# Kernel optimization log

Measured on AMD Instinct MI355X. Metric: run time of the kernel, lower is better.

The kernel has to match this reference:

```python
import jax, jax.numpy as jnp
import numpy as np
from jax import lax

N = 25600      # total nodes = G * T
E = 204800     # edges (before self loops)
IN_CH = 6
HID = 64
HEADS = 4
G = 512        # graphs per batch
T = 50         # sequence length (node_time in [0, T))
OUT = 30       # prediction_horizon * 3
NEG_SLOPE = 0.2
BN_EPS = 1e-5


def _gat(x, src, dst, W, a_src, a_dst, b, heads, outc):
    # PyG GATConv (concat=True): h = x W reshaped to (N, H, C)
    n = x.shape[0]
    h = (x @ W).reshape(n, heads, outc)
    # edge scores: leaky_relu(a_src . h_src + a_dst . h_dst), softmax over incoming edges of dst
    e = jax.nn.leaky_relu((h * a_src).sum(-1)[src] + (h * a_dst).sum(-1)[dst], NEG_SLOPE)  # (E, H)
    m = jax.ops.segment_max(e, dst, num_segments=n)
    ex = jnp.exp(e - m[dst])
    denom = jax.ops.segment_sum(ex, dst, num_segments=n)
    alpha = ex / denom[dst]
    out = jax.ops.segment_sum(alpha[:, :, None] * h[src], dst, num_segments=n)  # (N, H, C)
    return out.reshape(n, heads * outc) + b


def _bn_eval(x, g, b):
    # BatchNorm in eval with running_mean=0, running_var=1
    return g * (x * (1.0 / np.float32(np.sqrt(1.0 + BN_EPS)))) + b


def setup_inputs() -> dict:
    ks = jax.random.split(jax.random.key(0), 16)
    s = 0.1
    d = {}
    d["x"] = jax.random.normal(ks[0], (N, IN_CH), jnp.float32)
    d["edge_index"] = jax.random.randint(ks[1], (2, E), 0, N)
    idx = jnp.arange(N)
    d["batch"] = idx // T       # each graph has exactly T nodes
    d["node_time"] = idx % T
    d["W1"] = jax.random.normal(ks[2], (IN_CH, HEADS * HID), jnp.float32) * s
    d["att_src1"] = jax.random.normal(ks[3], (HEADS, HID), jnp.float32) * s
    d["att_dst1"] = jax.random.normal(ks[4], (HEADS, HID), jnp.float32) * s
    d["b1"] = jnp.zeros((HEADS * HID,), jnp.float32)
    d["g1"] = jnp.ones((HEADS * HID,), jnp.float32)
    d["be1"] = jnp.zeros((HEADS * HID,), jnp.float32)
    d["W2"] = jax.random.normal(ks[5], (HEADS * HID, HID), jnp.float32) * s
    d["att_src2"] = jax.random.normal(ks[6], (1, HID), jnp.float32) * s
    d["att_dst2"] = jax.random.normal(ks[7], (1, HID), jnp.float32) * s
    d["b2"] = jnp.zeros((HID,), jnp.float32)
    d["g2"] = jnp.ones((HID,), jnp.float32)
    d["be2"] = jnp.zeros((HID,), jnp.float32)
    d["Wih"] = jax.random.normal(ks[8], (4 * HID, HID), jnp.float32) * s
    d["Whh"] = jax.random.normal(ks[9], (4 * HID, HID), jnp.float32) * s
    d["bih"] = jnp.zeros((4 * HID,), jnp.float32)
    d["bhh"] = jnp.zeros((4 * HID,), jnp.float32)
    d["Wfc"] = jax.random.normal(ks[10], (HID, OUT), jnp.float32) * s
    d["bfc"] = jnp.zeros((OUT,), jnp.float32)
    return d


def reference(x, edge_index, batch, node_time, W1, att_src1, att_dst1, b1, g1, be1,
              W2, att_src2, att_dst2, b2, g2, be2, Wih, Whh, bih, bhh, Wfc, bfc):
    loops = jnp.arange(N)
    src = jnp.concatenate([edge_index[0], loops])  # GATConv adds self loops
    dst = jnp.concatenate([edge_index[1], loops])
    h = jax.nn.elu(_bn_eval(_gat(x, src, dst, W1, att_src1, att_dst1, b1, HEADS, HID), g1, be1))
    h = jax.nn.elu(_bn_eval(_gat(h, src, dst, W2, att_src2, att_dst2, b2, 1, HID), g2, be2))
    # vectorized replacement of the per-node python scatter loop
    x_seq = jnp.zeros((G, T, HID), h.dtype).at[batch, node_time].set(h)

    def step(carry, xt):
        hh, cc = carry
        gates = xt @ Wih.T + bih + hh @ Whh.T + bhh
        i, f, gg, o = jnp.split(gates, 4, axis=-1)
        cc = jax.nn.sigmoid(f) * cc + jax.nn.sigmoid(i) * jnp.tanh(gg)
        hh = jax.nn.sigmoid(o) * jnp.tanh(cc)
        return (hh, cc), None

    init = (jnp.zeros((G, HID), h.dtype), jnp.zeros((G, HID), h.dtype))
    (hn, _), _ = lax.scan(step, init, x_seq.transpose(1, 0, 2))  # scan over time
    return hn @ Wfc + bfc  # (G, 30)
```

## Files before the change

### kernel.cpp

```cpp
#include <hip/hip_runtime.h>

#define N_NODES 25600
#define N_EDGES 204800
#define EE (N_EDGES + N_NODES)
#define IN_CH 6
#define HID 64
#define HEADS 4
#define G_GRAPHS 512
#define T_STEPS 50
#define OUT_DIM 30
#define NEG_SLOPE 0.2f
#define BN_INV 0.9999950000374997f

__device__ __forceinline__ float lrelu_(float x){ return x > 0.f ? x : NEG_SLOPE * x; }
__device__ __forceinline__ float elu_(float x){ return x > 0.f ? x : __expf(x) - 1.f; }
__device__ __forceinline__ float sigmoid_(float x){ return 1.f / (1.f + __expf(-x)); }

__global__ void count_k(const int* __restrict__ ei, int* __restrict__ counts){
    int e = blockIdx.x * 256 + threadIdx.x;
    if (e >= EE) return;
    int dst = (e < N_EDGES) ? ei[N_EDGES + e] : (e - N_EDGES);
    atomicAdd(&counts[dst], 1);
}

__global__ void scan_k(const int* __restrict__ counts, int* __restrict__ row_ptr,
                       int* __restrict__ cursor){
    __shared__ int part[1024];
    int t = threadIdx.x;
    const int CH = N_NODES / 1024;
    int base = t * CH;
    int s = 0;
    for (int i = 0; i < CH; i++) s += counts[base + i];
    part[t] = s;
    __syncthreads();
    for (int off = 1; off < 1024; off <<= 1){
        int v = (t >= off) ? part[t - off] : 0;
        __syncthreads();
        part[t] += v;
        __syncthreads();
    }
    int run = (t > 0) ? part[t - 1] : 0;
    for (int i = 0; i < CH; i++){
        int cv = counts[base + i];
        row_ptr[base + i] = run;
        cursor[base + i]  = run;
        run += cv;
    }
    if (t == 1023) row_ptr[N_NODES] = run;
}

__global__ void scatter_k(const int* __restrict__ ei, int* __restrict__ cursor,
                          int* __restrict__ ssrc){
    int e = blockIdx.x * 256 + threadIdx.x;
    if (e >= EE) return;
    int src, dst;
    if (e < N_EDGES){ src = ei[e]; dst = ei[N_EDGES + e]; }
    else            { src = dst = e - N_EDGES; }
    int pos = atomicAdd(&cursor[dst], 1);
    ssrc[pos] = src;
}

__global__ void gat1_tr(const float* __restrict__ x, const float* __restrict__ W1,
                        const float* __restrict__ asw, const float* __restrict__ adw,
                        float* __restrict__ h1_pre, float* __restrict__ as1,
                        float* __restrict__ ad1){
    __shared__ float w[IN_CH * 256];
    int tid = threadIdx.x;
    for (int i = tid; i < IN_CH * 256; i += 256) w[i] = W1[i];
    __syncthreads();
    int wv = tid >> 6, lane = tid & 63;
    int n = blockIdx.x * 4 + wv;
    float xv[IN_CH];
    #pragma unroll
    for (int k = 0; k < IN_CH; k++) xv[k] = x[n * IN_CH + k];
    float sA[4], sD[4];
    #pragma unroll
    for (int h = 0; h < 4; h++){
        int col = h * 64 + lane;
        float acc = 0.f;
        #pragma unroll
        for (int k = 0; k < IN_CH; k++) acc += xv[k] * w[k * 256 + col];
        h1_pre[n * 256 + col] = acc;
        sA[h] = acc * asw[col];
        sD[h] = acc * adw[col];
    }
    #pragma unroll
    for (int h = 0; h < 4; h++){
        #pragma unroll
        for (int off = 32; off; off >>= 1){
            sA[h] += __shfl_xor(sA[h], off);
            sD[h] += __shfl_xor(sD[h], off);
        }
    }
    if (lane == 0){
        *(float4*)&as1[n * 4] = make_float4(sA[0], sA[1], sA[2], sA[3]);
        *(float4*)&ad1[n * 4] = make_float4(sD[0], sD[1], sD[2], sD[3]);
    }
}

__global__ void gat1_agg(const float* __restrict__ h1_pre, const float* __restrict__ as1,
                         const float* __restrict__ ad1, const int* __restrict__ row_ptr,
                         const int* __restrict__ ssrc,
                         const float* __restrict__ b1, const float* __restrict__ g1,
                         const float* __restrict__ be1, float* __restrict__ h1_act){
    int wv = threadIdx.x >> 6, lane = threadIdx.x & 63;
    int n = blockIdx.x * 4 + wv;
    int s0 = row_ptr[n], s1 = row_ptr[n + 1];
    float4 adn = *(const float4*)&ad1[n * 4];
    float d0 = 0.f, d1 = 0.f, d2 = 0.f, d3 = 0.f;
    float a0 = 0.f, a1 = 0.f, a2 = 0.f, a3 = 0.f;
    for (int j = s0; j < s1; j++){
        int s = ssrc[j];
        float4 as = *(const float4*)&as1[s * 4];
        float e0 = __expf(lrelu_(as.x + adn.x));
        float e1 = __expf(lrelu_(as.y + adn.y));
        float e2 = __expf(lrelu_(as.z + adn.z));
        float e3 = __expf(lrelu_(as.w + adn.w));
        d0 += e0; d1 += e1; d2 += e2; d3 += e3;
        const float* hp = h1_pre + (size_t)s * 256;
        a0 += e0 * hp[lane];
        a1 += e1 * hp[64 + lane];
        a2 += e2 * hp[128 + lane];
        a3 += e3 * hp[192 + lane];
    }
    float accs[4] = {a0 / d0, a1 / d1, a2 / d2, a3 / d3};
    #pragma unroll
    for (int h = 0; h < 4; h++){
        int col = h * 64 + lane;
        float v = accs[h] + b1[col];
        v = g1[col] * (v * BN_INV) + be1[col];
        h1_act[(size_t)n * 256 + col] = elu_(v);
    }
}

#define TM 64
#define KT 32
#define APAD 4
__global__ __launch_bounds__(256) void gat2_tr(const float* __restrict__ h1_act,
                        const float* __restrict__ W2,
                        const float* __restrict__ asw, const float* __restrict__ adw,
                        float* __restrict__ h2_pre, float* __restrict__ as2,
                        float* __restrict__ ad2){
    __shared__ float As[TM][KT + APAD];
    __shared__ float Bs[KT][64];
    int tx = threadIdx.x;
    int rg = tx >> 4;
    int cg = tx & 15;
    int r0 = rg * 4, c0 = cg * 4;
    int rowBase = blockIdx.x * TM;
    float acc[4][4] = {};
    for (int k0 = 0; k0 < 256; k0 += KT){
        #pragma unroll
        for (int it = 0; it < 2; it++){
            int i = tx + it * 256;
            int row = i >> 3;
            int c4  = (i & 7) * 4;
            *(float4*)&As[row][c4] =
                *(const float4*)(h1_act + (size_t)(rowBase + row) * 256 + k0 + c4);
        }
        #pragma unroll
        for (int it = 0; it < 2; it++){
            int i = tx + it * 256;
            int row = i >> 4;
            int c4  = (i & 15) * 4;
            *(float4*)&Bs[row][c4] = *(const float4*)(W2 + (size_t)(k0 + row) * 64 + c4);
        }
        __syncthreads();
        #pragma unroll
        for (int kq = 0; kq < KT; kq += 4){
            float4 b0 = *(float4*)&Bs[kq + 0][c0];
            float4 b1v = *(float4*)&Bs[kq + 1][c0];
            float4 b2v = *(float4*)&Bs[kq + 2][c0];
            float4 b3 = *(float4*)&Bs[kq + 3][c0];
            #pragma unroll
            for (int i = 0; i < 4; i++){
                float4 a = *(float4*)&As[r0 + i][kq];
                acc[i][0] += a.x * b0.x + a.y * b1v.x + a.z * b2v.x + a.w * b3.x;
                acc[i][1] += a.x * b0.y + a.y * b1v.y + a.z * b2v.y + a.w * b3.y;
                acc[i][2] += a.x * b0.z + a.y * b1v.z + a.z * b2v.z + a.w * b3.z;
                acc[i][3] += a.x * b0.w + a.y * b1v.w + a.z * b2v.w + a.w * b3.w;
            }
        }
        __syncthreads();
    }
    float aw0 = asw[c0], aw1 = asw[c0+1], aw2 = asw[c0+2], aw3 = asw[c0+3];
    float dw0 = adw[c0], dw1 = adw[c0+1], dw2 = adw[c0+2], dw3 = adw[c0+3];
    #pragma unroll
    for (int i = 0; i < 4; i++){
        int row = rowBase + r0 + i;
        *(float4*)(h2_pre + (size_t)row * 64 + c0) =
            make_float4(acc[i][0], acc[i][1], acc[i][2], acc[i][3]);
        float sA = acc[i][0]*aw0 + acc[i][1]*aw1 + acc[i][2]*aw2 + acc[i][3]*aw3;
        float sD = acc[i][0]*dw0 + acc[i][1]*dw1 + acc[i][2]*dw2 + acc[i][3]*dw3;
        #pragma unroll
        for (int off = 8; off; off >>= 1){
            sA += __shfl_xor(sA, off);
            sD += __shfl_xor(sD, off);
        }
        if (cg == 0){ as2[row] = sA; ad2[row] = sD; }
    }
}

__global__ void gat2_agg(const float* __restrict__ h2_pre, const float* __restrict__ as2,
                         const float* __restrict__ ad2, const int* __restrict__ row_ptr,
                         const int* __restrict__ ssrc,
                         const float* __restrict__ b2, const float* __restrict__ g2,
                         const float* __restrict__ be2,
                         const int* __restrict__ batch, const int* __restrict__ ntime,
                         float* __restrict__ xseq){
    int wv = threadIdx.x >> 6, lane = threadIdx.x & 63;
    int n = blockIdx.x * 4 + wv;
    int s0 = row_ptr[n], s1 = row_ptr[n + 1];
    float adn = ad2[n];
    float denom = 0.f, acc = 0.f;
    for (int j = s0; j < s1; j++){
        int s = ssrc[j];
        float e = __expf(lrelu_(as2[s] + adn));
        denom += e;
        acc += e * h2_pre[(size_t)s * 64 + lane];
    }
    float v = acc / denom + b2[lane];
    v = g2[lane] * (v * BN_INV) + be2[lane];
    v = elu_(v);
    int pos = batch[n] * T_STEPS + ntime[n];
    xseq[(size_t)pos * 64 + lane] = v;
}

__global__ __launch_bounds__(256, 2) void lstm_k(const float* __restrict__ xseq,
        const float* __restrict__ Wih, const float* __restrict__ Whh,
        const float* __restrict__ bih, const float* __restrict__ bhh,
        const float* __restrict__ Wfc, const float* __restrict__ bfc,
        float* __restrict__ out){
    int g = blockIdx.x;
    int j = threadIdx.x;
    __shared__ float4 xt4[16];
    __shared__ float4 h4[16];
    __shared__ float gates[256];
    float4 wih[16], whh[16];
    const float4* Wr = (const float4*)(Wih + j * 64);
    const float4* Hr = (const float4*)(Whh + j * 64);
    #pragma unroll
    for (int k = 0; k < 16; k++){ wih[k] = Wr[k]; whh[k] = Hr[k]; }
    float bsum = bih[j] + bhh[j];
    float c = 0.f;
    if (j < 16) h4[j] = make_float4(0.f, 0.f, 0.f, 0.f);
    __syncthreads();
    const float4* xg = (const float4*)(xseq + (size_t)g * T_STEPS * 64);
    for (int t = 0; t < T_STEPS; t++){
        if (j < 16) xt4[j] = xg[t * 16 + j];
        __syncthreads();
        float acc = bsum;
        #pragma unroll
        for (int k = 0; k < 16; k++){
            float4 xv = xt4[k]; float4 wv = wih[k];
            acc += wv.x * xv.x; acc += wv.y * xv.y;
            acc += wv.z * xv.z; acc += wv.w * xv.w;
            float4 hv = h4[k]; float4 wh = whh[k];
            acc += wh.x * hv.x; acc += wh.y * hv.y;
            acc += wh.z * hv.z; acc += wh.w * hv.w;
        }
        gates[j] = acc;
        __syncthreads();
        if (j < 64){
            float iv = gates[j], fv = gates[64 + j], gv = gates[128 + j], ov = gates[192 + j];
            c = sigmoid_(fv) * c + sigmoid_(iv) * tanhf(gv);
            float hn = sigmoid_(ov) * tanhf(c);
            ((float*)h4)[j] = hn;
        }
        __syncthreads();
    }
    if (j < OUT_DIM){
        float acc = bfc[j];
        const float* hf = (const float*)h4;
        #pragma unroll
        for (int k = 0; k < 64; k++) acc += hf[k] * Wfc[k * OUT_DIM + j];
        out[g * OUT_DIM + j] = acc;
    }
}

extern "C" void kernel_launch(void* const* d_in, const int* in_sizes, int n_in,
                              void* d_out, int out_size, void* d_ws, size_t ws_size,
                              hipStream_t stream){
    const float* x    = (const float*)d_in[0];
    const int*   ei   = (const int*)  d_in[1];
    const int*   batch= (const int*)  d_in[2];
    const int*   ntime= (const int*)  d_in[3];
    const float* W1   = (const float*)d_in[4];
    const float* as1w = (const float*)d_in[5];
    const float* ad1w = (const float*)d_in[6];
    const float* b1   = (const float*)d_in[7];
    const float* g1   = (const float*)d_in[8];
    const float* be1  = (const float*)d_in[9];
    const float* W2   = (const float*)d_in[10];
    const float* as2w = (const float*)d_in[11];
    const float* ad2w = (const float*)d_in[12];
    const float* b2   = (const float*)d_in[13];
    const float* g2   = (const float*)d_in[14];
    const float* be2  = (const float*)d_in[15];
    const float* Wih  = (const float*)d_in[16];
    const float* Whh  = (const float*)d_in[17];
    const float* bih  = (const float*)d_in[18];
    const float* bhh  = (const float*)d_in[19];
    const float* Wfc  = (const float*)d_in[20];
    const float* bfc  = (const float*)d_in[21];
    float* out = (float*)d_out;

    char* w = (char*)d_ws;
    auto alloc = [&](size_t bytes)->char*{
        char* p = w;
        w += (bytes + 255) & ~size_t(255);
        return p;
    };
    float* h1_pre = (float*)alloc((size_t)N_NODES * 256 * 4);
    float* h1_act = (float*)alloc((size_t)N_NODES * 256 * 4);
    float* h2_pre = (float*)alloc((size_t)N_NODES * 64 * 4);
    float* xseq   = (float*)alloc((size_t)G_GRAPHS * T_STEPS * 64 * 4);
    float* as1    = (float*)alloc((size_t)N_NODES * 4 * 4);
    float* ad1    = (float*)alloc((size_t)N_NODES * 4 * 4);
    float* as2    = (float*)alloc((size_t)N_NODES * 4);
    float* ad2    = (float*)alloc((size_t)N_NODES * 4);
    int* counts   = (int*)alloc((size_t)N_NODES * 4);
    int* row_ptr  = (int*)alloc((size_t)(N_NODES + 1) * 4);
    int* cursor   = (int*)alloc((size_t)N_NODES * 4);
    int* ssrc     = (int*)alloc((size_t)EE * 4);

    hipMemsetAsync(counts, 0, (size_t)N_NODES * 4, stream);
    count_k  <<<(EE + 255) / 256, 256, 0, stream>>>(ei, counts);
    scan_k   <<<1, 1024, 0, stream>>>(counts, row_ptr, cursor);
    scatter_k<<<(EE + 255) / 256, 256, 0, stream>>>(ei, cursor, ssrc);
    gat1_tr  <<<N_NODES / 4, 256, 0, stream>>>(x, W1, as1w, ad1w, h1_pre, as1, ad1);
    gat1_agg <<<N_NODES / 4, 256, 0, stream>>>(h1_pre, as1, ad1, row_ptr, ssrc, b1, g1, be1, h1_act);
    gat2_tr  <<<N_NODES / TM, 256, 0, stream>>>(h1_act, W2, as2w, ad2w, h2_pre, as2, ad2);
    gat2_agg <<<N_NODES / 4, 256, 0, stream>>>(h2_pre, as2, ad2, row_ptr, ssrc, b2, g2, be2, batch, ntime, xseq);
    lstm_k   <<<G_GRAPHS, 256, 0, stream>>>(xseq, Wih, Whh, bih, bhh, Wfc, bfc, out);
}
```

Measured before the change: 315.4 us.

## Hoist LSTM input projection into a separate batched GEMM kernel

Computes x_t·Wih^T plus both biases for all timesteps up front in a tiled shared-memory GEMM and writes the result into the reused h1_pre buffer. The recurrent kernel then only does the Whh product each step, which removes one barrier per step and half the per-step FMAs and weight registers. In exchange it adds an extra kernel launch and a write and read of a 25600x256 float intermediate. Sigmoid also switches to a fast division.

Result: no change. 320.0 us (+1.4%).

```diff
diff --git a/kernel.cpp b/kernel.cpp
--- a/kernel.cpp
+++ b/kernel.cpp
@@ -14,7 +14,7 @@
 
 __device__ __forceinline__ float lrelu_(float x){ return x > 0.f ? x : NEG_SLOPE * x; }
 __device__ __forceinline__ float elu_(float x){ return x > 0.f ? x : __expf(x) - 1.f; }
-__device__ __forceinline__ float sigmoid_(float x){ return 1.f / (1.f + __expf(-x)); }
+__device__ __forceinline__ float sigmoid_(float x){ return __fdividef(1.f, 1.f + __expf(-x)); }
 
 __global__ void count_k(const int* __restrict__ ei, int* __restrict__ counts){
     int e = blockIdx.x * 256 + threadIdx.x;
@@ -226,35 +226,79 @@
     xseq[(size_t)pos * 64 + lane] = v;
 }
 
-__global__ __launch_bounds__(256, 2) void lstm_k(const float* __restrict__ xseq,
-        const float* __restrict__ Wih, const float* __restrict__ Whh,
-        const float* __restrict__ bih, const float* __restrict__ bhh,
-        const float* __restrict__ Wfc, const float* __restrict__ bfc,
-        float* __restrict__ out){
+__global__ __launch_bounds__(256) void xproj_k(const float* __restrict__ xseq,
+        const float* __restrict__ Wih, const float* __restrict__ bih,
+        const float* __restrict__ bhh, float* __restrict__ xproj){
+    __shared__ float As[64][68];
+    __shared__ float Bs[64][64];
+    int tx = threadIdx.x;
+    int bx = blockIdx.x;
+    int m0 = (bx >> 2) * 64, n0 = (bx & 3) * 64;
+    #pragma unroll
+    for (int it = 0; it < 4; it++){
+        int i = tx + it * 256;
+        int r = i >> 4, c4 = (i & 15) * 4;
+        *(float4*)&As[r][c4] = *(const float4*)(xseq + (size_t)(m0 + r) * 64 + c4);
+    }
+    #pragma unroll
+    for (int it = 0; it < 4; it++){
+        int i = tx + it * 256;
+        int n = i & 63, k4 = (i >> 6) * 4;
+        float4 w = *(const float4*)(Wih + (size_t)(n0 + n) * 64 + k4);
+        Bs[k4 + 0][n] = w.x; Bs[k4 + 1][n] = w.y;
+        Bs[k4 + 2][n] = w.z; Bs[k4 + 3][n] = w.w;
+    }
+    __syncthreads();
+    int rg = tx >> 4, cg = tx & 15;
+    int r0 = rg * 4, c0 = cg * 4;
+    float acc[4][4] = {};
+    #pragma unroll
+    for (int k4 = 0; k4 < 16; k4++){
+        int k = k4 * 4;
+        float4 b0 = *(float4*)&Bs[k + 0][c0];
+        float4 b1v = *(float4*)&Bs[k + 1][c0];
+        float4 b2v = *(float4*)&Bs[k + 2][c0];
+        float4 b3 = *(float4*)&Bs[k + 3][c0];
+        #pragma unroll
+        for (int i = 0; i < 4; i++){
+            float4 a = *(float4*)&As[r0 + i][k];
+            acc[i][0] += a.x * b0.x + a.y * b1v.x + a.z * b2v.x + a.w * b3.x;
+            acc[i][1] += a.x * b0.y + a.y * b1v.y + a.z * b2v.y + a.w * b3.y;
+            acc[i][2] += a.x * b0.z + a.y * b1v.z + a.z * b2v.z + a.w * b3.z;
+            acc[i][3] += a.x * b0.w + a.y * b1v.w + a.z * b2v.w + a.w * b3.w;
+        }
+    }
+    float bb0 = bih[n0 + c0 + 0] + bhh[n0 + c0 + 0];
+    float bb1 = bih[n0 + c0 + 1] + bhh[n0 + c0 + 1];
+    float bb2 = bih[n0 + c0 + 2] + bhh[n0 + c0 + 2];
+    float bb3 = bih[n0 + c0 + 3] + bhh[n0 + c0 + 3];
+    #pragma unroll
+    for (int i = 0; i < 4; i++){
+        int row = m0 + r0 + i;
+        *(float4*)(xproj + (size_t)row * 256 + n0 + c0) =
+            make_float4(acc[i][0] + bb0, acc[i][1] + bb1, acc[i][2] + bb2, acc[i][3] + bb3);
+    }
+}
+
+__global__ __launch_bounds__(256, 2) void lstm3_k(const float* __restrict__ xproj,
+        const float* __restrict__ Whh, const float* __restrict__ Wfc,
+        const float* __restrict__ bfc, float* __restrict__ out){
     int g = blockIdx.x;
     int j = threadIdx.x;
-    __shared__ float4 xt4[16];
     __shared__ float4 h4[16];
     __shared__ float gates[256];
-    float4 wih[16], whh[16];
-    const float4* Wr = (const float4*)(Wih + j * 64);
-    const float4* Hr = (const float4*)(Whh + j * 64);
-    #pragma unroll
-    for (int k = 0; k < 16; k++){ wih[k] = Wr[k]; whh[k] = Hr[k]; }
-    float bsum = bih[j] + bhh[j];
+    float4 whh[16];
+    const float4* Hr = (const float4*)(Whh + (size_t)j * 64);
+    #pragma unroll
+    for (int k = 0; k < 16; k++) whh[k] = Hr[k];
     float c = 0.f;
     if (j < 16) h4[j] = make_float4(0.f, 0.f, 0.f, 0.f);
     __syncthreads();
-    const float4* xg = (const float4*)(xseq + (size_t)g * T_STEPS * 64);
+    const float* xp = xproj + (size_t)g * T_STEPS * 256;
     for (int t = 0; t < T_STEPS; t++){
-        if (j < 16) xt4[j] = xg[t * 16 + j];
-        __syncthreads();
-        float acc = bsum;
+        float acc = xp[t * 256 + j];
         #pragma unroll
         for (int k = 0; k < 16; k++){
-            float4 xv = xt4[k]; float4 wv = wih[k];
-            acc += wv.x * xv.x; acc += wv.y * xv.y;
-            acc += wv.z * xv.z; acc += wv.w * xv.w;
             float4 hv = h4[k]; float4 wh = whh[k];
             acc += wh.x * hv.x; acc += wh.y * hv.y;
             acc += wh.z * hv.z; acc += wh.w * hv.w;
@@ -323,6 +367,7 @@
     int* row_ptr  = (int*)alloc((size_t)(N_NODES + 1) * 4);
     int* cursor   = (int*)alloc((size_t)N_NODES * 4);
     int* ssrc     = (int*)alloc((size_t)EE * 4);
+    float* xproj  = h1_pre;
 
     hipMemsetAsync(counts, 0, (size_t)N_NODES * 4, stream);
     count_k  <<<(EE + 255) / 256, 256, 0, stream>>>(ei, counts);
@@ -332,5 +377,6 @@
     gat1_agg <<<N_NODES / 4, 256, 0, stream>>>(h1_pre, as1, ad1, row_ptr, ssrc, b1, g1, be1, h1_act);
     gat2_tr  <<<N_NODES / TM, 256, 0, stream>>>(h1_act, W2, as2w, ad2w, h2_pre, as2, ad2);
     gat2_agg <<<N_NODES / 4, 256, 0, stream>>>(h2_pre, as2, ad2, row_ptr, ssrc, b2, g2, be2, batch, ntime, xseq);
-    lstm_k   <<<G_GRAPHS, 256, 0, stream>>>(xseq, Wih, Whh, bih, bhh, Wfc, bfc, out);
-}
+    xproj_k  <<<(N_NODES / 64) * 4, 256, 0, stream>>>(xseq, Wih, bih, bhh, xproj);
+    lstm3_k  <<<G_GRAPHS, 256, 0, stream>>>(xproj, Whh, Wfc, bfc, out);
+}
```
